# Optimization experiments

Measured on AMD Instinct MI355X. Metric: run time of the kernel, lower is better.

Reference implementation:

```python
import jax, jax.numpy as jnp
import numpy as np

SEQ, B, IN, H = 512, 64, 1024, 1024


def setup_inputs() -> dict:
    key = jax.random.key(0)
    k0, k1, k2, k3, k4 = jax.random.split(key, 5)
    stdv = 1.0 / np.sqrt(H)
    Xt = jax.random.normal(k0, (SEQ, B, IN), dtype=jnp.float32)
    # layer 0: concat(x[IN], h0[H]) -> H ; layer 1: concat(y0[H], h1[H]) -> H
    W0 = jax.random.uniform(k1, (H, IN + H), dtype=jnp.float32, minval=-stdv, maxval=stdv)
    b0 = jax.random.uniform(k2, (H,), dtype=jnp.float32, minval=-stdv, maxval=stdv)
    W1 = jax.random.uniform(k3, (H, H + H), dtype=jnp.float32, minval=-stdv, maxval=stdv)
    b1 = jax.random.uniform(k4, (H,), dtype=jnp.float32, minval=-stdv, maxval=stdv)
    return {"Xt": Xt, "W0": W0, "b0": b0, "W1": W1, "b1": b1}


def reference(Xt, W0, b0, W1, b1):
    # Concatenated-gate stacked tanh RNN (n_states=1), seq-major layout [S,B,F].
    Bsz = Xt.shape[1]
    h0 = jnp.zeros((Bsz, W0.shape[0]), dtype=Xt.dtype)
    h1 = jnp.zeros((Bsz, W1.shape[0]), dtype=Xt.dtype)

    def step(carry, x):
        h0, h1 = carry
        h0n = jnp.tanh(jnp.concatenate([x, h0], axis=-1) @ W0.T + b0)
        h1n = jnp.tanh(jnp.concatenate([h0n, h1], axis=-1) @ W1.T + b1)
        return (h0n, h1n), h1n

    (_, _), Y = jax.lax.scan(step, (h0, h1), Xt)
    return Y  # [SEQ, B, H] — stacked top-layer outputs (stack_output=True)
```

## Files before the change

kernel.cpp:

```cpp
#include <hip/hip_runtime.h>


typedef unsigned short ushort_t;
typedef unsigned int uint32;
typedef __attribute__((ext_vector_type(4))) unsigned int u32x4;
typedef __attribute__((ext_vector_type(4))) float f32x4;
typedef __attribute__((ext_vector_type(8))) __bf16 bfrag;

__device__ __forceinline__ f32x4 mfma_bf16(u32x4 a, u32x4 b, f32x4 c) {
  return __builtin_amdgcn_mfma_f32_16x16x32_bf16(
      __builtin_bit_cast(bfrag, a), __builtin_bit_cast(bfrag, b), c, 0, 0, 0);
}

__device__ __forceinline__ uint32 bf16rne(float f) {
  uint32 u = __builtin_bit_cast(uint32, f);
  return (u + 0x7fffu + ((u >> 16) & 1u)) >> 16;
}

__device__ __forceinline__ uint32 cvt_pk(float lo, float hi) {
  uint32 r;
  asm("v_cvt_pk_bf16_f32 %0, %1, %2" : "=v"(r) : "v"(lo), "v"(hi));
  return r;
}
__device__ __forceinline__ u32x4 pack8(f32x4 a, f32x4 b) {
  u32x4 r;
  r.x = cvt_pk(a.x, a.y);
  r.y = cvt_pk(a.z, a.w);
  r.z = cvt_pk(b.x, b.y);
  r.w = cvt_pk(b.z, b.w);
  return r;
}

template <int BOFF>
__device__ __forceinline__ void ld16(u32x4& d, const ushort_t* base) {
  asm volatile("global_load_dwordx4 %0, %1, off offset:%c2 sc0"
               : "=v"(d) : "v"(base), "i"(BOFF) : "memory");
}

#define LOADB(BUF, AP, KOFF)                 \
  ld16<(KOFF) * 2 + 0>(BUF[0], AP);          \
  ld16<(KOFF) * 2 + 64>(BUF[1], AP);         \
  ld16<(KOFF) * 2 + 128>(BUF[2], AP);        \
  ld16<(KOFF) * 2 + 192>(BUF[3], AP);        \
  ld16<(KOFF) * 2 + 256>(BUF[4], AP);        \
  ld16<(KOFF) * 2 + 320>(BUF[5], AP);        \
  ld16<(KOFF) * 2 + 384>(BUF[6], AP);        \
  ld16<(KOFF) * 2 + 448>(BUF[7], AP);

__device__ __forceinline__ int poll_ge(const int* p, int tgt, int* ab) {
  for (int it = 0;; ++it) {
    int v;
    asm volatile("global_load_dword %0, %1, off sc0 sc1\n\ts_waitcnt vmcnt(0)"
                 : "=v"(v) : "v"(p) : "memory");
    if (v >= tgt) return 0;
    asm volatile("s_sleep 4" ::: "memory");
    if ((it & 255) == 255) {
      int a;
      asm volatile("global_load_dword %0, %1, off sc0 sc1\n\ts_waitcnt vmcnt(0)"
                   : "=v"(a) : "v"(ab) : "memory");
      if (a) return 1;
      if (it > (1 << 18)) {
        int one = 1;
        asm volatile("global_store_dword %0, %1, off sc0 sc1\n\ts_waitcnt vmcnt(0)"
                     :: "v"(ab), "v"(one) : "memory");
        return 1;
      }
    }
  }
}

__global__ void rnn_init(int* c) {
  for (int k = threadIdx.x; k < 772; k += 256) {
    int z = 0;
    asm volatile("global_store_dword %0, %1, off sc0 sc1"
                 :: "v"(c + k), "v"(z) : "memory");
  }
  asm volatile("s_waitcnt vmcnt(0)" ::: "memory");
}

__global__ __launch_bounds__(512) void rnn_main(
    const float* __restrict__ Xt, const float* __restrict__ W0,
    const float* __restrict__ b0, const float* __restrict__ W1,
    const float* __restrict__ b1, float* __restrict__ Y,
    ushort_t* hbuf, int* cnt) {
  __shared__ float part[2][4][16][17];
  __shared__ int s_slot;

  const int tid = threadIdx.x;
  const int wave = tid >> 6;
  const int lane = tid & 63;
  const int ln15 = lane & 15;
  const int lq = lane >> 4;
  const int n = wave & 3;
  const bool fin = wave < 4;

  uint32 xcc;
  asm("s_getreg_b32 %0, hwreg(HW_REG_XCC_ID)" : "=s"(xcc));
  const int xcd = xcc & 7;

  int* slotp  = cnt + xcd * 96;
  int* ctr0   = cnt + xcd * 96 + 32;
  int* ctr1   = cnt + xcd * 96 + 64;
  int* abortp = cnt + 768;

  if (tid == 0) {
    int one = 1, old;
    asm volatile("global_atomic_add %0, %1, %2, off sc0 sc1\n\ts_waitcnt vmcnt(0)"
                 : "=v"(old) : "v"(slotp), "v"(one) : "memory");
    s_slot = old & 31;
  }
  __syncthreads();
  const int slot = s_slot;
  const bool isL1 = slot >= 16;
  const int F0 = (slot & 15) * 64;
  const int fcol = F0 + n * 16 + ln15;
  const int row8 = ln15 & 7;

  const int kh = isL1 ? (fin ? 0 : 1) : (fin ? 1 : 0);
  const float* Wsrc = isL1 ? W1 : W0;

  u32x4 bw[32];
  {
    const float* wp = Wsrc + (size_t)fcol * 2048 + kh * 1024 + lq * 8;
#pragma unroll
    for (int j = 0; j < 32; ++j) {
      f32x4 w0 = *(const f32x4*)(wp + j * 32);
      f32x4 w1 = *(const f32x4*)(wp + j * 32 + 4);
      bw[j] = pack8(w0, w1);
    }
  }
  const float bia = fin ? (isL1 ? b1 : b0)[fcol] : 0.f;

  ushort_t* h0b = hbuf + (size_t)xcd * 40960;
  ushort_t* h1b = h0b + 24576;

  auto gemm_h = [&](const ushort_t* hsrc) -> f32x4 {
    f32x4 a = {0.f, 0.f, 0.f, 0.f};
    const ushort_t* ap = hsrc + row8 * 1024 + lq * 8;
    u32x4 fa[8], fb[8];
    LOADB(fa, ap, 0);
    LOADB(fb, ap, 256);
    asm volatile("s_waitcnt vmcnt(8)" ::: "memory");
    __builtin_amdgcn_sched_barrier(0);
#pragma unroll
    for (int j = 0; j < 8; ++j) a = mfma_bf16(fa[j], bw[j], a);
    LOADB(fa, ap, 512);
    asm volatile("s_waitcnt vmcnt(8)" ::: "memory");
    __builtin_amdgcn_sched_barrier(0);
#pragma unroll
    for (int j = 0; j < 8; ++j) a = mfma_bf16(fb[j], bw[8 + j], a);
    LOADB(fb, ap, 768);
    asm volatile("s_waitcnt vmcnt(8)" ::: "memory");
    __builtin_amdgcn_sched_barrier(0);
#pragma unroll
    for (int j = 0; j < 8; ++j) a = mfma_bf16(fa[j], bw[16 + j], a);
    asm volatile("s_waitcnt vmcnt(0)" ::: "memory");
    __builtin_amdgcn_sched_barrier(0);
#pragma unroll
    for (int j = 0; j < 8; ++j) a = mfma_bf16(fb[j], bw[24 + j], a);
    return a;
  };

  auto gemm_x = [&](int t) -> f32x4 {
    f32x4 a = {0.f, 0.f, 0.f, 0.f};
    const float* xp = Xt + ((size_t)t * 64 + xcd * 8 + row8) * 1024 + lq * 8;
#pragma unroll
    for (int j = 0; j < 32; ++j) {
      f32x4 x0 = *(const f32x4*)(xp + j * 32);
      f32x4 x1 = *(const f32x4*)(xp + j * 32 + 4);
      a = mfma_bf16(pack8(x0, x1), bw[j], a);
    }
    return a;
  };

  for (int t = 0; t < 512; ++t) {
    const int buf = t & 1;
    f32x4 acc = {0.f, 0.f, 0.f, 0.f};
    uint32 pf0 = 0, pf1 = 0;

    if (!isL1) {
      if (fin) {
        if (wave == 0) {
          if (t >= 1) poll_ge(ctr0, 16 * t, abortp);
          if (t >= 2) poll_ge(ctr1, 16 * (t - 2), abortp);
        }
      } else {
        {
          int tn = t < 511 ? t + 1 : 511;
          const char* pfp = (const char*)(Xt + ((size_t)tn * 64 + xcd * 8) * 1024)
                            + n * 8192 + lane * 128;
          asm volatile("global_load_dword %0, %1, off" : "=v"(pf0) : "v"(pfp));
          asm volatile("global_load_dword %0, %1, off offset:64" : "=v"(pf1) : "v"(pfp));
        }
        acc = gemm_x(t);
#pragma unroll
        for (int r = 0; r < 4; ++r) part[buf][n][lq * 4 + r][ln15] = acc[r];
      }
    } else {
      if (wave == 0) {
        if (t >= 1) poll_ge(ctr1, 16 * t, abortp);
        poll_ge(ctr0, 16 * (t + 1), abortp);
      }
    }
    __syncthreads();

    if (!isL1) {
      if (fin && t >= 1) acc = gemm_h(h0b + ((t - 1) % 3) * 8192);
    } else {
      if (fin) {
        acc = gemm_h(h0b + (t % 3) * 8192);
      } else {
        if (t >= 1) acc = gemm_h(h1b + ((t - 1) & 1) * 8192);
#pragma unroll
        for (int r = 0; r < 4; ++r) part[buf][n][lq * 4 + r][ln15] = acc[r];
      }
    }
    if (!fin) asm volatile("" :: "v"(pf0), "v"(pf1));
    __syncthreads();

    if (fin) {
      float o[4];
#pragma unroll
      for (int r = 0; r < 4; ++r) {
        float s = acc[r] + part[buf][n][lq * 4 + r][ln15] + bia;
        float ax = fabsf(s);
        float e = __expf(2.f * ax);
        float rr = 1.f - 2.f * __builtin_amdgcn_rcpf(e + 1.f);
        o[r] = copysignf(rr, s);
      }
      if (lq < 2) {
        ushort_t* hd = (isL1 ? h1b + (t & 1) * 8192 : h0b + (t % 3) * 8192)
                       + (lq * 4) * 1024 + fcol;
#pragma unroll
        for (int r = 0; r < 4; ++r) {
          uint32 hv = bf16rne(o[r]);
          asm volatile("global_store_short %0, %1, off sc0"
                       :: "v"(hd + r * 1024), "v"(hv) : "memory");
        }
        if (isL1) {
          float* yd = Y + ((size_t)t * 64 + xcd * 8 + lq * 4) * 1024 + fcol;
#pragma unroll
          for (int r = 0; r < 4; ++r) yd[r * 1024] = o[r];
        }
      }
      asm volatile("s_waitcnt vmcnt(0)" ::: "memory");
    }
    __syncthreads();

    if (tid == 0) {
      int one = 1;
      int* cp = isL1 ? ctr1 : ctr0;
      asm volatile("global_atomic_add %0, %1, off sc1" :: "v"(cp), "v"(one) : "memory");
    }
  }
}

extern "C" void kernel_launch(void* const* d_in, const int* in_sizes, int n_in,
                              void* d_out, int out_size, void* d_ws, size_t ws_size,
                              hipStream_t stream) {
  const float* Xt = (const float*)d_in[0];
  const float* W0 = (const float*)d_in[1];
  const float* b0 = (const float*)d_in[2];
  const float* W1 = (const float*)d_in[3];
  const float* b1 = (const float*)d_in[4];
  float* Y = (float*)d_out;

  int* cnt = (int*)d_ws;
  ushort_t* hbuf = (ushort_t*)((char*)d_ws + 4096);

  rnn_init<<<1, 256, 0, stream>>>(cnt);
  rnn_main<<<256, 512, 0, stream>>>(Xt, W0, b0, W1, b1, Y, hbuf, cnt);
}
```

Baseline: 6.625 ms.

## Replace atomic step counters with per-block flag arrays polled by lanes

Inter-block synchronisation switches from shared atomic-add counters to one flag per block, written with a plain store of the step index. Wave 0 polls all 16 producer flags of each layer in parallel across lanes and waits until every lane's condition holds. This removes atomic contention on a single counter and shortens the poll sleep. The cost is a larger flag workspace, which moves the hidden-state buffer offset, and a slightly changed wait structure in which layer-0 x-gemm waves no longer sit behind a polling branch.

```diff
diff --git a/kernel.cpp b/kernel.cpp
--- a/kernel.cpp
+++ b/kernel.cpp
@@ -47,30 +47,8 @@
   ld16<(KOFF) * 2 + 384>(BUF[6], AP);        \
   ld16<(KOFF) * 2 + 448>(BUF[7], AP);
 
-__device__ __forceinline__ int poll_ge(const int* p, int tgt, int* ab) {
-  for (int it = 0;; ++it) {
-    int v;
-    asm volatile("global_load_dword %0, %1, off sc0 sc1\n\ts_waitcnt vmcnt(0)"
-                 : "=v"(v) : "v"(p) : "memory");
-    if (v >= tgt) return 0;
-    asm volatile("s_sleep 4" ::: "memory");
-    if ((it & 255) == 255) {
-      int a;
-      asm volatile("global_load_dword %0, %1, off sc0 sc1\n\ts_waitcnt vmcnt(0)"
-                   : "=v"(a) : "v"(ab) : "memory");
-      if (a) return 1;
-      if (it > (1 << 18)) {
-        int one = 1;
-        asm volatile("global_store_dword %0, %1, off sc0 sc1\n\ts_waitcnt vmcnt(0)"
-                     :: "v"(ab), "v"(one) : "memory");
-        return 1;
-      }
-    }
-  }
-}
-
 __global__ void rnn_init(int* c) {
-  for (int k = threadIdx.x; k < 772; k += 256) {
+  for (int k = threadIdx.x; k < 8193; k += 256) {
     int z = 0;
     asm volatile("global_store_dword %0, %1, off sc0 sc1"
                  :: "v"(c + k), "v"(z) : "memory");
@@ -98,15 +76,13 @@
   asm("s_getreg_b32 %0, hwreg(HW_REG_XCC_ID)" : "=s"(xcc));
   const int xcd = xcc & 7;
 
-  int* slotp  = cnt + xcd * 96;
-  int* ctr0   = cnt + xcd * 96 + 32;
-  int* ctr1   = cnt + xcd * 96 + 64;
-  int* abortp = cnt + 768;
+  int* fbase  = cnt + xcd * 1024;
+  int* abortp = cnt + 8192;
 
   if (tid == 0) {
     int one = 1, old;
     asm volatile("global_atomic_add %0, %1, %2, off sc0 sc1\n\ts_waitcnt vmcnt(0)"
-                 : "=v"(old) : "v"(slotp), "v"(one) : "memory");
+                 : "=v"(old) : "v"(fbase), "v"(one) : "memory");
     s_slot = old & 31;
   }
   __syncthreads();
@@ -115,6 +91,11 @@
   const int F0 = (slot & 15) * 64;
   const int fcol = F0 + n * 16 + ln15;
   const int row8 = ln15 & 7;
+
+  const int* myf = (lane < 16) ? (fbase + 16 + ln15 * 16)
+                  : (lane < 32) ? (fbase + 528 + ln15 * 16)
+                                : (fbase + 16);
+  int* myflag = fbase + (isL1 ? 528 : 16) + (slot & 15) * 16;
 
   const int kh = isL1 ? (fin ? 0 : 1) : (fin ? 1 : 0);
   const float* Wsrc = isL1 ? W1 : W0;
@@ -178,29 +159,42 @@
     f32x4 acc = {0.f, 0.f, 0.f, 0.f};
     uint32 pf0 = 0, pf1 = 0;
 
-    if (!isL1) {
-      if (fin) {
-        if (wave == 0) {
-          if (t >= 1) poll_ge(ctr0, 16 * t, abortp);
-          if (t >= 2) poll_ge(ctr1, 16 * (t - 2), abortp);
+    if (wave == 0) {
+      const int tA = isL1 ? t + 1 : t;
+      const int tB = isL1 ? t : t - 2;
+      const int tgt = (lane < 16) ? tA : (lane < 32) ? tB : -2000000000;
+      if (tA > 0) {
+        for (int it = 0;; ++it) {
+          int v;
+          asm volatile("global_load_dword %0, %1, off sc0 sc1\n\ts_waitcnt vmcnt(0)"
+                       : "=v"(v) : "v"(myf) : "memory");
+          if (__all(v >= tgt)) break;
+          asm volatile("s_sleep 2" ::: "memory");
+          if ((it & 255) == 255) {
+            int a;
+            asm volatile("global_load_dword %0, %1, off sc0 sc1\n\ts_waitcnt vmcnt(0)"
+                         : "=v"(a) : "v"(abortp) : "memory");
+            if (a) break;
+            if (it > (1 << 18)) {
+              int one = 1;
+              asm volatile("global_store_dword %0, %1, off sc0 sc1\n\ts_waitcnt vmcnt(0)"
+                           :: "v"(abortp), "v"(one) : "memory");
+              break;
+            }
+          }
         }
-      } else {
-        {
-          int tn = t < 511 ? t + 1 : 511;
-          const char* pfp = (const char*)(Xt + ((size_t)tn * 64 + xcd * 8) * 1024)
-                            + n * 8192 + lane * 128;
-          asm volatile("global_load_dword %0, %1, off" : "=v"(pf0) : "v"(pfp));
-          asm volatile("global_load_dword %0, %1, off offset:64" : "=v"(pf1) : "v"(pfp));
-        }
-        acc = gemm_x(t);
-#pragma unroll
-        for (int r = 0; r < 4; ++r) part[buf][n][lq * 4 + r][ln15] = acc[r];
-      }
-    } else {
-      if (wave == 0) {
-        if (t >= 1) poll_ge(ctr1, 16 * t, abortp);
-        poll_ge(ctr0, 16 * (t + 1), abortp);
-      }
+      }
+    } else if (!isL1 && !fin) {
+      {
+        int tn = t < 511 ? t + 1 : 511;
+        const char* pfp = (const char*)(Xt + ((size_t)tn * 64 + xcd * 8) * 1024)
+                          + n * 8192 + lane * 128;
+        asm volatile("global_load_dword %0, %1, off" : "=v"(pf0) : "v"(pfp));
+        asm volatile("global_load_dword %0, %1, off offset:64" : "=v"(pf1) : "v"(pfp));
+      }
+      acc = gemm_x(t);
+#pragma unroll
+      for (int r = 0; r < 4; ++r) part[buf][n][lq * 4 + r][ln15] = acc[r];
     }
     __syncthreads();
 
@@ -248,9 +242,9 @@
     __syncthreads();
 
     if (tid == 0) {
-      int one = 1;
-      int* cp = isL1 ? ctr1 : ctr0;
-      asm volatile("global_atomic_add %0, %1, off sc1" :: "v"(cp), "v"(one) : "memory");
+      int val = t + 1;
+      asm volatile("global_store_dword %0, %1, off sc0 sc1"
+                   :: "v"(myflag), "v"(val) : "memory");
     }
   }
 }
@@ -266,7 +260,7 @@
   float* Y = (float*)d_out;
 
   int* cnt = (int*)d_ws;
-  ushort_t* hbuf = (ushort_t*)((char*)d_ws + 4096);
+  ushort_t* hbuf = (ushort_t*)((char*)d_ws + 36864);
 
   rnn_init<<<1, 256, 0, stream>>>(cnt);
   rnn_main<<<256, 512, 0, stream>>>(Xt, W0, b0, W1, b1, Y, hbuf, cnt);
```

Measured after the change: 6.311 ms. 1.05x faster.
